# Optimization experiments

Hardware: AMD Instinct MI355X
Metric: run time of the kernel (lower is better)

The kernel has to match this reference:

```python
import jax, jax.numpy as jnp
import numpy as np

N_NODES = 100_000
N_EDGES = 1_600_000
N_RELS = 16
D_IN = 128
D_OUT = 64


def setup_inputs() -> dict:
    key = jax.random.key(0)
    k_feat, k_w, k_src, k_dst, k_et = jax.random.split(key, 5)
    feat = jax.random.normal(k_feat, (N_NODES, D_IN), dtype=jnp.float32)
    weight = jax.random.normal(k_w, (N_RELS, D_IN, D_OUT), dtype=jnp.float32)
    src = jax.random.randint(k_src, (N_EDGES,), 0, N_NODES, dtype=jnp.int32)
    dst = jax.random.randint(k_dst, (N_EDGES,), 0, N_NODES, dtype=jnp.int32)
    etypes = jnp.sort(jax.random.randint(k_et, (N_EDGES,), 0, N_RELS, dtype=jnp.int32))
    return {"feat": feat, "weight": weight, "src": src, "dst": dst, "etypes": etypes}


def reference(feat, weight, src, dst, etypes):
    # RGCN gather-mm: message m_e = feat[src_e] @ W[etype_e]; out_v = sum_{e: dst_e = v} m_e
    # Efficient form: project all nodes with all relation weights (dense GEMM, small R),
    # then gather the (etype, src) slice per edge and segment-sum into destinations.
    proj = jnp.einsum('nd,rde->rne', feat, weight)          # [R, N, d_out]
    msg = proj[etypes, src]                                  # [E, d_out] irregular gather
    out = jax.ops.segment_sum(msg, dst, num_segments=feat.shape[0])  # [N, d_out] scatter-sum
    return out
```

## Files before the change

kernel.cpp:

```cpp
#include <hip/hip_runtime.h>
#include <hip/hip_bf16.h>


#define NTHREADS 256
#define TM 64
#define CH 2560

typedef __attribute__((ext_vector_type(8))) __bf16 bf16x8;
typedef __attribute__((ext_vector_type(4))) float f32x4;

__global__ void cvt_w_kernel(const float* __restrict__ w,
                             __bf16* __restrict__ o, int total) {
    int idx = blockIdx.x * 256 + threadIdx.x;
    if (idx >= total) return;
    int r = idx >> 13;
    int rem = idx & 8191;
    int k = rem >> 6;
    int n = rem & 63;
    o[(r << 13) + (n << 7) + k] = (__bf16)w[idx];
}

__global__ __launch_bounds__(NTHREADS)
void proj_all_kernel(const float* __restrict__ feat, const __bf16* __restrict__ wtb,
                     const unsigned char* __restrict__ usedb,
                     int N, int R, __bf16* __restrict__ projb) {
    __shared__ __bf16 Wt[2][64 * 136];
    __shared__ unsigned used_l[16 * 32];

    int t = threadIdx.x;
    int wave = t >> 6, lane = t & 63;
    int q = lane >> 4, m = lane & 15;
    long blk0 = (long)blockIdx.x * 128;
    long node0 = blk0 + wave * 32;

    for (int c = t; c < R * 32; c += NTHREADS) {
        int rr = c >> 5, i = c & 31;
        used_l[rr * 32 + i] = *(const unsigned*)(usedb + (size_t)rr * N + blk0 + i * 4);
    }

    bf16x8 a[2][4];
    #pragma unroll
    for (int mt = 0; mt < 2; mt++) {
        long nd = node0 + mt * 16 + m;
        if (nd > N - 1) nd = N - 1;
        const float* arow = feat + nd * 128;
        #pragma unroll
        for (int ks = 0; ks < 4; ks++) {
            float4 fa = *(const float4*)(arow + ks * 32 + q * 8);
            float4 fb = *(const float4*)(arow + ks * 32 + q * 8 + 4);
            bf16x8 v;
            v[0] = (__bf16)fa.x; v[1] = (__bf16)fa.y; v[2] = (__bf16)fa.z; v[3] = (__bf16)fa.w;
            v[4] = (__bf16)fb.x; v[5] = (__bf16)fb.y; v[6] = (__bf16)fb.z; v[7] = (__bf16)fb.w;
            a[mt][ks] = v;
        }
    }

    {
        const __bf16* wg = wtb;
        #pragma unroll
        for (int i = 0; i < 4; i++) {
            int c = t + i * 256;
            int n = c >> 4, kc = c & 15;
            *(bf16x8*)(&Wt[0][n * 136 + kc * 8]) = *(const bf16x8*)(wg + n * 128 + kc * 8);
        }
    }
    asm volatile("s_waitcnt lgkmcnt(0)" ::: "memory");
    __builtin_amdgcn_s_barrier();
    __builtin_amdgcn_sched_barrier(0);

    for (int r = 0; r < R; r++) {
        int cur = r & 1, nxt = cur ^ 1;
        bool pf = (r + 1 < R);

        bf16x8 wreg[4];
        if (pf) {
            const __bf16* wg = wtb + ((size_t)(r + 1) << 13);
            #pragma unroll
            for (int i = 0; i < 4; i++) {
                int c = t + i * 256;
                int n = c >> 4, kc = c & 15;
                wreg[i] = *(const bf16x8*)(wg + n * 128 + kc * 8);
            }
        }

        f32x4 acc[2][4] = {};
        #pragma unroll
        for (int ks = 0; ks < 4; ks++) {
            bf16x8 b0 = *(const bf16x8*)(&Wt[cur][(0 * 16 + m) * 136 + ks * 32 + q * 8]);
            bf16x8 b1 = *(const bf16x8*)(&Wt[cur][(1 * 16 + m) * 136 + ks * 32 + q * 8]);
            bf16x8 b2 = *(const bf16x8*)(&Wt[cur][(2 * 16 + m) * 136 + ks * 32 + q * 8]);
            bf16x8 b3 = *(const bf16x8*)(&Wt[cur][(3 * 16 + m) * 136 + ks * 32 + q * 8]);
            #pragma unroll
            for (int mt = 0; mt < 2; mt++) {
                acc[mt][0] = __builtin_amdgcn_mfma_f32_16x16x32_bf16(a[mt][ks], b0, acc[mt][0], 0, 0, 0);
                acc[mt][1] = __builtin_amdgcn_mfma_f32_16x16x32_bf16(a[mt][ks], b1, acc[mt][1], 0, 0, 0);
                acc[mt][2] = __builtin_amdgcn_mfma_f32_16x16x32_bf16(a[mt][ks], b2, acc[mt][2], 0, 0, 0);
                acc[mt][3] = __builtin_amdgcn_mfma_f32_16x16x32_bf16(a[mt][ks], b3, acc[mt][3], 0, 0, 0);
            }
        }

        #pragma unroll
        for (int mt = 0; mt < 2; mt++) {
            unsigned g = used_l[r * 32 + ((wave * 32 + mt * 16 + q * 4) >> 2)];
            #pragma unroll
            for (int reg = 0; reg < 4; reg++) {
                long nd = node0 + mt * 16 + q * 4 + reg;
                if (nd < N && ((g >> (reg * 8)) & 1)) {
                    union { unsigned long long u; __bf16 h[4]; } pk;
                    pk.h[0] = (__bf16)acc[mt][0][reg];
                    pk.h[1] = (__bf16)acc[mt][1][reg];
                    pk.h[2] = (__bf16)acc[mt][2][reg];
                    pk.h[3] = (__bf16)acc[mt][3][reg];
                    *(unsigned long long*)(projb + ((size_t)r * N + nd) * 64 + m * 4) = pk.u;
                }
            }
        }

        if (pf) {
            #pragma unroll
            for (int i = 0; i < 4; i++) {
                int c = t + i * 256;
                int n = c >> 4, kc = c & 15;
                *(bf16x8*)(&Wt[nxt][n * 136 + kc * 8]) = wreg[i];
            }
            asm volatile("s_waitcnt lgkmcnt(0)" ::: "memory");
            __builtin_amdgcn_s_barrier();
            __builtin_amdgcn_sched_barrier(0);
        }
    }
}

__global__ __launch_bounds__(1024)
void bucket_scatter(const int* __restrict__ dst, const int* __restrict__ src,
                    const int* __restrict__ etypes, int E, int N, int NB, int STRIDE,
                    int* __restrict__ bcnt, int* __restrict__ items,
                    unsigned char* __restrict__ usedb) {
    __shared__ int lh[1024], lb[1024];
    int t = threadIdx.x;
    lh[t] = 0;
    __syncthreads();
    long base = (long)blockIdx.x * 8192;
    int bs[8], it[8];
    #pragma unroll
    for (int i = 0; i < 8; i++) {
        long e = base + t + 1024 * i;
        if (e < E) {
            int d = dst[e];
            int bkt = d >> 7;
            bs[i] = bkt;
            int pair = etypes[e] * N + src[e];
            it[i] = ((d & 127) << 24) | pair;
            usedb[pair] = 1;
            atomicAdd(&lh[bkt], 1);
        } else bs[i] = -1;
    }
    __syncthreads();
    for (int bb = t; bb < NB; bb += 1024) {
        int c = lh[bb];
        lb[bb] = c ? atomicAdd(&bcnt[bb], c) : 0;
        lh[bb] = 0;
    }
    __syncthreads();
    #pragma unroll
    for (int i = 0; i < 8; i++) {
        if (bs[i] >= 0) {
            int pos = lb[bs[i]] + atomicAdd(&lh[bs[i]], 1);
            if (pos < STRIDE)
                items[(size_t)bs[i] * STRIDE + pos] = it[i];
        }
    }
}

__global__ __launch_bounds__(512)
void bucket_reduce(const int* __restrict__ bcnt, const int* __restrict__ items,
                   int STRIDE, const __bf16* __restrict__ projb, int N,
                   float* __restrict__ out) {
    __shared__ int h[128], sc[128], cur[128];
    __shared__ int its[CH];
    int b = blockIdx.x, t = threadIdx.x;
    int cnt = bcnt[b]; if (cnt > STRIDE) cnt = STRIDE;
    const int* bitems = items + (size_t)b * STRIDE;
    int sub = t >> 3, c8 = t & 7;

    float acc[2][8] = {};

    for (int c0 = 0; c0 < cnt; c0 += CH) {
        int n = cnt - c0; if (n > CH) n = CH;

        if (t < 128) h[t] = 0;
        __syncthreads();

        int my[CH / 512];
        int dl[CH / 512];
        #pragma unroll
        for (int i = 0; i < CH / 512; i++) {
            int k = t + i * 512;
            if (k < n) {
                my[i] = bitems[c0 + k];
                dl[i] = ((unsigned)my[i]) >> 24;
                atomicAdd(&h[dl[i]], 1);
            } else dl[i] = -1;
        }
        __syncthreads();

        if (t < 128) sc[t] = h[t];
        __syncthreads();
        for (int s = 1; s < 128; s <<= 1) {
            int add = (t >= s && t < 128) ? sc[t - s] : 0;
            __syncthreads();
            if (t < 128) sc[t] += add;
            __syncthreads();
        }
        if (t < 128) cur[t] = sc[t] - h[t];
        __syncthreads();

        #pragma unroll
        for (int i = 0; i < CH / 512; i++) {
            if (dl[i] >= 0) {
                int pos = atomicAdd(&cur[dl[i]], 1);
                its[pos] = my[i] & 0xFFFFFF;
            }
        }
        __syncthreads();

        #pragma unroll
        for (int idx = 0; idx < 2; idx++) {
            int d = sub + idx * 64;
            int s = sc[d] - h[d];
            int e = sc[d];
            int k = s;
            for (; k + 1 < e; k += 2) {
                int p0 = its[k], p1 = its[k + 1];
                bf16x8 v0 = *(const bf16x8*)(projb + (size_t)p0 * 64 + c8 * 8);
                bf16x8 v1 = *(const bf16x8*)(projb + (size_t)p1 * 64 + c8 * 8);
                #pragma unroll
                for (int i = 0; i < 8; i++) acc[idx][i] += (float)v0[i] + (float)v1[i];
            }
            if (k < e) {
                int p = its[k];
                bf16x8 v0 = *(const bf16x8*)(projb + (size_t)p * 64 + c8 * 8);
                #pragma unroll
                for (int i = 0; i < 8; i++) acc[idx][i] += (float)v0[i];
            }
        }
        __syncthreads();
    }

    #pragma unroll
    for (int idx = 0; idx < 2; idx++) {
        long v = (long)b * 128 + sub + idx * 64;
        if (v < N) {
            float* orow = out + (size_t)v * 64;
            #pragma unroll
            for (int i = 0; i < 8; i++) {
                int cp = c8 * 8 + i;
                orow[(cp & 3) * 16 + (cp >> 2)] = acc[idx][i];
            }
        }
    }
}

__global__ __launch_bounds__(NTHREADS)
void rgcn_atomic(const float* __restrict__ feat, const float* __restrict__ weight,
                 const int* __restrict__ src, const int* __restrict__ dst,
                 const int* __restrict__ etypes, int E,
                 float* __restrict__ out) {
    __shared__ __bf16 Wt[64 * 136];
    int b = blockIdx.x;
    int e0 = b * TM;
    int t = threadIdx.x;
    int wave = t >> 6, lane = t & 63;
    int q = lane >> 4, m = lane & 15;
    int wbase = e0 + wave * 16;
    int last = e0 + TM - 1; if (last > E - 1) last = E - 1;
    int rmin = etypes[e0];
    int rmax = etypes[last];
    int em = wbase + m;
    bool rowok = em < E;
    int ei = rowok ? em : E - 1;
    int my_et = rowok ? etypes[em] : -1;
    const float* arow = feat + (long)src[ei] * 128;
    bf16x8 a[4];
    #pragma unroll
    for (int ks = 0; ks < 4; ks++) {
        float4 fa = *(const float4*)(arow + ks * 32 + q * 8);
        float4 fb = *(const float4*)(arow + ks * 32 + q * 8 + 4);
        bf16x8 v;
        v[0] = (__bf16)fa.x; v[1] = (__bf16)fa.y;
        v[2] = (__bf16)fa.z; v[3] = (__bf16)fa.w;
        v[4] = (__bf16)fb.x; v[5] = (__bf16)fb.y;
        v[6] = (__bf16)fb.z; v[7] = (__bf16)fb.w;
        a[ks] = v;
    }
    f32x4 acc0 = {0.f, 0.f, 0.f, 0.f};
    f32x4 acc1 = {0.f, 0.f, 0.f, 0.f};
    f32x4 acc2 = {0.f, 0.f, 0.f, 0.f};
    f32x4 acc3 = {0.f, 0.f, 0.f, 0.f};
    for (int r = rmin; r <= rmax; ++r) {
        if (r != rmin) __syncthreads();
        const float* wg = weight + (r << 13);
        for (int p = t; p < 4096; p += NTHREADS) {
            int n = p & 63, kh = p >> 6;
            float w0 = wg[(kh * 2) * 64 + n];
            float w1 = wg[(kh * 2 + 1) * 64 + n];
            union { unsigned u; __bf16 h[2]; } pk;
            pk.h[0] = (__bf16)w0; pk.h[1] = (__bf16)w1;
            *(unsigned*)&Wt[n * 136 + kh * 2] = pk.u;
        }
        __syncthreads();
        bool on = (my_et == r);
        #pragma unroll
        for (int ks = 0; ks < 4; ks++) {
            bf16x8 af = a[ks];
            if (!on) {
                #pragma unroll
                for (int j = 0; j < 8; j++) af[j] = (__bf16)0.f;
            }
            bf16x8 b0 = *(const bf16x8*)(&Wt[(0 * 16 + m) * 136 + ks * 32 + q * 8]);
            bf16x8 b1 = *(const bf16x8*)(&Wt[(1 * 16 + m) * 136 + ks * 32 + q * 8]);
            bf16x8 b2 = *(const bf16x8*)(&Wt[(2 * 16 + m) * 136 + ks * 32 + q * 8]);
            bf16x8 b3 = *(const bf16x8*)(&Wt[(3 * 16 + m) * 136 + ks * 32 + q * 8]);
            acc0 = __builtin_amdgcn_mfma_f32_16x16x32_bf16(af, b0, acc0, 0, 0, 0);
            acc1 = __builtin_amdgcn_mfma_f32_16x16x32_bf16(af, b1, acc1, 0, 0, 0);
            acc2 = __builtin_amdgcn_mfma_f32_16x16x32_bf16(af, b2, acc2, 0, 0, 0);
            acc3 = __builtin_amdgcn_mfma_f32_16x16x32_bf16(af, b3, acc3, 0, 0, 0);
        }
    }
    #pragma unroll
    for (int reg = 0; reg < 4; reg++) {
        int er = wbase + q * 4 + reg;
        if (er < E) {
            float* orow = out + (long)dst[er] * 64;
            unsafeAtomicAdd(orow + 0 * 16 + m, acc0[reg]);
            unsafeAtomicAdd(orow + 1 * 16 + m, acc1[reg]);
            unsafeAtomicAdd(orow + 2 * 16 + m, acc2[reg]);
            unsafeAtomicAdd(orow + 3 * 16 + m, acc3[reg]);
        }
    }
}

extern "C" void kernel_launch(void* const* d_in, const int* in_sizes, int n_in,
                              void* d_out, int out_size, void* d_ws, size_t ws_size,
                              hipStream_t stream) {
    const float* feat   = (const float*)d_in[0];
    const float* weight = (const float*)d_in[1];
    const int*   src    = (const int*)d_in[2];
    const int*   dst    = (const int*)d_in[3];
    const int*   etypes = (const int*)d_in[4];
    float* out = (float*)d_out;

    int nfeat = in_sizes[0];
    int nw    = in_sizes[1];
    int E     = in_sizes[2];
    int N     = nfeat / 128;
    int R     = nw >> 13;
    int NB    = (N + 127) >> 7;

    int avg = (int)(((long)E + NB - 1) / NB);
    int STRIDE = ((avg * 2 + 63) / 64) * 64;
    if (STRIDE < 1024) STRIDE = 1024;

    size_t o = 0;
    auto take = [&](size_t bytes) { size_t r = o; o = (o + bytes + 255) & ~(size_t)255; return r; };
    size_t o_bcnt  = take((size_t)NB * 4);
    size_t o_usedb = take((size_t)R * N);
    size_t o_items = take((size_t)NB * STRIDE * 4);
    size_t o_wtb   = take((size_t)nw * 2);
    size_t o_projb = take((size_t)R * N * 64 * 2);
    size_t need = o;

    bool fast = (ws_size >= need) && (NB <= 1024) && ((size_t)R * N < (1u << 24)) && (R <= 16);

    if (fast) {
        char* ws = (char*)d_ws;
        int* bcnt  = (int*)(ws + o_bcnt);
        unsigned char* usedb = (unsigned char*)(ws + o_usedb);
        int* items = (int*)(ws + o_items);
        __bf16* wtb   = (__bf16*)(ws + o_wtb);
        __bf16* projb = (__bf16*)(ws + o_projb);

        int cgrid = (int)(((long)E + 8191) / 8192);

        hipMemsetAsync(bcnt, 0, (o_usedb - o_bcnt) + (size_t)R * N, stream);
        bucket_scatter<<<cgrid, 1024, 0, stream>>>(dst, src, etypes, E, N, NB, STRIDE,
                                                   bcnt, items, usedb);
        cvt_w_kernel<<<(nw + 255) / 256, 256, 0, stream>>>(weight, wtb, nw);

        proj_all_kernel<<<(N + 127) / 128, NTHREADS, 0, stream>>>(feat, wtb, usedb, N, R, projb);
        bucket_reduce<<<NB, 512, 0, stream>>>(bcnt, items, STRIDE, projb, N, out);
    } else {
        hipMemsetAsync(d_out, 0, (size_t)out_size * sizeof(float), stream);
        int mgrid = (E + TM - 1) / TM;
        rgcn_atomic<<<mgrid, NTHREADS, 0, stream>>>(feat, weight, src, dst, etypes, E, out);
    }
}
```

Before: 240.6 us.

## Fuse bucket scatter into projection kernel and drop used-pair mask

Merges the edge bucketing pass and the all-relation projection GEMM into one launch, with separate block ranges doing each job so they run concurrently. The used-(etype,src) byte mask is removed, so the projection now writes every node for every relation instead of skipping unused pairs. This saves a kernel launch, the mask memset and the byte-mask writes and reads, at the cost of writing the full R×N×64 bf16 projection to memory. Scatter blocks now use 256 threads with 2048 edges each instead of 1024 threads with 8192 edges.

```diff
diff --git a/kernel.cpp b/kernel.cpp
--- a/kernel.cpp
+++ b/kernel.cpp
@@ -5,6 +5,7 @@
 #define NTHREADS 256
 #define TM 64
 #define CH 2560
+#define SC_EPB 2048
 
 typedef __attribute__((ext_vector_type(8))) __bf16 bf16x8;
 typedef __attribute__((ext_vector_type(4))) float f32x4;
@@ -21,22 +22,61 @@
 }
 
 __global__ __launch_bounds__(NTHREADS)
-void proj_all_kernel(const float* __restrict__ feat, const __bf16* __restrict__ wtb,
-                     const unsigned char* __restrict__ usedb,
-                     int N, int R, __bf16* __restrict__ projb) {
-    __shared__ __bf16 Wt[2][64 * 136];
-    __shared__ unsigned used_l[16 * 32];
-
+void fused_scatter_proj(const int* __restrict__ dst, const int* __restrict__ src,
+                        const int* __restrict__ etypes, int E, int N, int NB,
+                        int STRIDE, int SB,
+                        int* __restrict__ bcnt, int* __restrict__ items,
+                        const float* __restrict__ feat,
+                        const __bf16* __restrict__ wtb, int R,
+                        __bf16* __restrict__ projb) {
+    __shared__ __attribute__((aligned(16))) char smem[2 * 64 * 136 * 2];
+
+    int bid = blockIdx.x;
     int t = threadIdx.x;
+
+    if (bid < SB) {
+        int* lh = (int*)smem;
+        int* lb = ((int*)smem) + 1024;
+        for (int i = t; i < 1024; i += NTHREADS) lh[i] = 0;
+        __syncthreads();
+        long base = (long)bid * SC_EPB;
+        int bs[8], it[8];
+        #pragma unroll
+        for (int i = 0; i < 8; i++) {
+            long e = base + t + NTHREADS * i;
+            if (e < E) {
+                int d = dst[e];
+                int bkt = d >> 7;
+                bs[i] = bkt;
+                it[i] = ((d & 127) << 24) | (etypes[e] * N + src[e]);
+                atomicAdd(&lh[bkt], 1);
+            } else bs[i] = -1;
+        }
+        __syncthreads();
+        for (int bb = t; bb < NB; bb += NTHREADS) {
+            int c = lh[bb];
+            lb[bb] = c ? atomicAdd(&bcnt[bb], c) : 0;
+            lh[bb] = 0;
+        }
+        __syncthreads();
+        #pragma unroll
+        for (int i = 0; i < 8; i++) {
+            if (bs[i] >= 0) {
+                int pos = lb[bs[i]] + atomicAdd(&lh[bs[i]], 1);
+                if (pos < STRIDE)
+                    items[(size_t)bs[i] * STRIDE + pos] = it[i];
+            }
+        }
+        return;
+    }
+
+    __bf16* Wt0 = (__bf16*)smem;
+    __bf16* Wt1 = ((__bf16*)smem) + 64 * 136;
+
     int wave = t >> 6, lane = t & 63;
     int q = lane >> 4, m = lane & 15;
-    long blk0 = (long)blockIdx.x * 128;
+    long blk0 = (long)(bid - SB) * 128;
     long node0 = blk0 + wave * 32;
-
-    for (int c = t; c < R * 32; c += NTHREADS) {
-        int rr = c >> 5, i = c & 31;
-        used_l[rr * 32 + i] = *(const unsigned*)(usedb + (size_t)rr * N + blk0 + i * 4);
-    }
 
     bf16x8 a[2][4];
     #pragma unroll
@@ -61,7 +101,7 @@
         for (int i = 0; i < 4; i++) {
             int c = t + i * 256;
             int n = c >> 4, kc = c & 15;
-            *(bf16x8*)(&Wt[0][n * 136 + kc * 8]) = *(const bf16x8*)(wg + n * 128 + kc * 8);
+            *(bf16x8*)(&Wt0[n * 136 + kc * 8]) = *(const bf16x8*)(wg + n * 128 + kc * 8);
         }
     }
     asm volatile("s_waitcnt lgkmcnt(0)" ::: "memory");
@@ -69,7 +109,8 @@
     __builtin_amdgcn_sched_barrier(0);
 
     for (int r = 0; r < R; r++) {
-        int cur = r & 1, nxt = cur ^ 1;
+        __bf16* Wcur = (r & 1) ? Wt1 : Wt0;
+        __bf16* Wnxt = (r & 1) ? Wt0 : Wt1;
         bool pf = (r + 1 < R);
 
         bf16x8 wreg[4];
@@ -86,10 +127,10 @@
         f32x4 acc[2][4] = {};
         #pragma unroll
         for (int ks = 0; ks < 4; ks++) {
-            bf16x8 b0 = *(const bf16x8*)(&Wt[cur][(0 * 16 + m) * 136 + ks * 32 + q * 8]);
-            bf16x8 b1 = *(const bf16x8*)(&Wt[cur][(1 * 16 + m) * 136 + ks * 32 + q * 8]);
-            bf16x8 b2 = *(const bf16x8*)(&Wt[cur][(2 * 16 + m) * 136 + ks * 32 + q * 8]);
-            bf16x8 b3 = *(const bf16x8*)(&Wt[cur][(3 * 16 + m) * 136 + ks * 32 + q * 8]);
+            bf16x8 b0 = *(const bf16x8*)(&Wcur[(0 * 16 + m) * 136 + ks * 32 + q * 8]);
+            bf16x8 b1 = *(const bf16x8*)(&Wcur[(1 * 16 + m) * 136 + ks * 32 + q * 8]);
+            bf16x8 b2 = *(const bf16x8*)(&Wcur[(2 * 16 + m) * 136 + ks * 32 + q * 8]);
+            bf16x8 b3 = *(const bf16x8*)(&Wcur[(3 * 16 + m) * 136 + ks * 32 + q * 8]);
             #pragma unroll
             for (int mt = 0; mt < 2; mt++) {
                 acc[mt][0] = __builtin_amdgcn_mfma_f32_16x16x32_bf16(a[mt][ks], b0, acc[mt][0], 0, 0, 0);
@@ -101,11 +142,10 @@
 
         #pragma unroll
         for (int mt = 0; mt < 2; mt++) {
-            unsigned g = used_l[r * 32 + ((wave * 32 + mt * 16 + q * 4) >> 2)];
             #pragma unroll
             for (int reg = 0; reg < 4; reg++) {
                 long nd = node0 + mt * 16 + q * 4 + reg;
-                if (nd < N && ((g >> (reg * 8)) & 1)) {
+                if (nd < N) {
                     union { unsigned long long u; __bf16 h[4]; } pk;
                     pk.h[0] = (__bf16)acc[mt][0][reg];
                     pk.h[1] = (__bf16)acc[mt][1][reg];
@@ -121,52 +161,11 @@
             for (int i = 0; i < 4; i++) {
                 int c = t + i * 256;
                 int n = c >> 4, kc = c & 15;
-                *(bf16x8*)(&Wt[nxt][n * 136 + kc * 8]) = wreg[i];
+                *(bf16x8*)(&Wnxt[n * 136 + kc * 8]) = wreg[i];
             }
             asm volatile("s_waitcnt lgkmcnt(0)" ::: "memory");
             __builtin_amdgcn_s_barrier();
             __builtin_amdgcn_sched_barrier(0);
-        }
-    }
-}
-
-__global__ __launch_bounds__(1024)
-void bucket_scatter(const int* __restrict__ dst, const int* __restrict__ src,
-                    const int* __restrict__ etypes, int E, int N, int NB, int STRIDE,
-                    int* __restrict__ bcnt, int* __restrict__ items,
-                    unsigned char* __restrict__ usedb) {
-    __shared__ int lh[1024], lb[1024];
-    int t = threadIdx.x;
-    lh[t] = 0;
-    __syncthreads();
-    long base = (long)blockIdx.x * 8192;
-    int bs[8], it[8];
-    #pragma unroll
-    for (int i = 0; i < 8; i++) {
-        long e = base + t + 1024 * i;
-        if (e < E) {
-            int d = dst[e];
-            int bkt = d >> 7;
-            bs[i] = bkt;
-            int pair = etypes[e] * N + src[e];
-            it[i] = ((d & 127) << 24) | pair;
-            usedb[pair] = 1;
-            atomicAdd(&lh[bkt], 1);
-        } else bs[i] = -1;
-    }
-    __syncthreads();
-    for (int bb = t; bb < NB; bb += 1024) {
-        int c = lh[bb];
-        lb[bb] = c ? atomicAdd(&bcnt[bb], c) : 0;
-        lh[bb] = 0;
-    }
-    __syncthreads();
-    #pragma unroll
-    for (int i = 0; i < 8; i++) {
-        if (bs[i] >= 0) {
-            int pos = lb[bs[i]] + atomicAdd(&lh[bs[i]], 1);
-            if (pos < STRIDE)
-                items[(size_t)bs[i] * STRIDE + pos] = it[i];
         }
     }
 }
@@ -363,30 +362,28 @@
     size_t o = 0;
     auto take = [&](size_t bytes) { size_t r = o; o = (o + bytes + 255) & ~(size_t)255; return r; };
     size_t o_bcnt  = take((size_t)NB * 4);
-    size_t o_usedb = take((size_t)R * N);
     size_t o_items = take((size_t)NB * STRIDE * 4);
     size_t o_wtb   = take((size_t)nw * 2);
     size_t o_projb = take((size_t)R * N * 64 * 2);
     size_t need = o;
 
-    bool fast = (ws_size >= need) && (NB <= 1024) && ((size_t)R * N < (1u << 24)) && (R <= 16);
+    bool fast = (ws_size >= need) && (NB <= 1024) && ((size_t)R * N < (1u << 24));
 
     if (fast) {
         char* ws = (char*)d_ws;
         int* bcnt  = (int*)(ws + o_bcnt);
-        unsigned char* usedb = (unsigned char*)(ws + o_usedb);
         int* items = (int*)(ws + o_items);
         __bf16* wtb   = (__bf16*)(ws + o_wtb);
         __bf16* projb = (__bf16*)(ws + o_projb);
 
-        int cgrid = (int)(((long)E + 8191) / 8192);
-
-        hipMemsetAsync(bcnt, 0, (o_usedb - o_bcnt) + (size_t)R * N, stream);
-        bucket_scatter<<<cgrid, 1024, 0, stream>>>(dst, src, etypes, E, N, NB, STRIDE,
-                                                   bcnt, items, usedb);
+        int SB = (int)(((long)E + SC_EPB - 1) / SC_EPB);
+        int PT = (N + 127) / 128;
+
+        hipMemsetAsync(bcnt, 0, (size_t)NB * 4, stream);
         cvt_w_kernel<<<(nw + 255) / 256, 256, 0, stream>>>(weight, wtb, nw);
-
-        proj_all_kernel<<<(N + 127) / 128, NTHREADS, 0, stream>>>(feat, wtb, usedb, N, R, projb);
+        fused_scatter_proj<<<SB + PT, NTHREADS, 0, stream>>>(
+            dst, src, etypes, E, N, NB, STRIDE, SB, bcnt, items,
+            feat, wtb, R, projb);
         bucket_reduce<<<NB, 512, 0, stream>>>(bcnt, items, STRIDE, projb, N, out);
     } else {
         hipMemsetAsync(d_out, 0, (size_t)out_size * sizeof(float), stream);
```

New measurement: 247.5 us. 1.03x slower.
